# Performance work log

Measured on AMD Instinct MI355X. Metric: run time of the kernel, lower is better.

The kernel has to match this reference:

```python
import jax, jax.numpy as jnp
import numpy as np

B, S, D = 2, 2048, 2048
NH, NKV, HD = 32, 8, 64
RATIO = NH // NKV  # 4
EPS = 1e-6


def setup_inputs() -> dict:
    key = jax.random.key(0)
    ks = jax.random.split(key, 6)
    x = jax.random.normal(ks[0], (B, S, D), dtype=jnp.float32)
    # weights stored (in, out) so projection is x @ W
    wq = jax.random.normal(ks[1], (D, NH * HD), dtype=jnp.float32) * 0.02
    wk = jax.random.normal(ks[2], (D, NKV * HD), dtype=jnp.float32) * 0.02
    wv = jax.random.normal(ks[3], (D, NKV * HD), dtype=jnp.float32) * 0.02
    wo = jax.random.normal(ks[4], (NH * HD, D), dtype=jnp.float32) * 0.02
    q_scale = jnp.ones((HD,), dtype=jnp.float32)
    k_scale = jnp.ones((HD,), dtype=jnp.float32)
    # RoPE tables (S, HD): duplicated-half layout
    inv_freq = 1.0 / (10000.0 ** (np.arange(0, HD, 2, dtype=np.float32) / HD))
    t = np.arange(S, dtype=np.float32)
    freqs = np.outer(t, inv_freq)  # (S, HD/2)
    emb = np.concatenate([freqs, freqs], axis=-1)  # (S, HD)
    cos = jnp.asarray(np.cos(emb))
    sin = jnp.asarray(np.sin(emb))
    # causal mask: True above diagonal = masked
    mask = jnp.triu(jnp.ones((S, S), dtype=jnp.bool_), k=1)
    return {"x": x, "wq": wq, "wk": wk, "wv": wv, "wo": wo,
            "q_scale": q_scale, "k_scale": k_scale,
            "cos": cos, "sin": sin, "mask": mask}


def _rms_norm(x, scale):
    # Qwen3-compatible: compute in fp32, cast back
    idt = x.dtype
    xf = x.astype(jnp.float32)
    nx = xf * jax.lax.rsqrt(jnp.mean(xf * xf, axis=-1, keepdims=True) + EPS)
    return (nx * scale).astype(idt)


def _rope(x, cos, sin):
    # x: (b, h, s, hd); cos/sin: (s, hd)
    hd = x.shape[-1]
    x1, x2 = x[..., : hd // 2], x[..., hd // 2:]
    rot = jnp.concatenate([-x2, x1], axis=-1)
    return x * cos[None, None] + rot * sin[None, None]


def reference(x, wq, wk, wv, wo, q_scale, k_scale, cos, sin, mask):
    b, sl, _ = x.shape
    q = (x @ wq).reshape(b, sl, NH, HD).transpose(0, 2, 1, 3)    # (b, nh, s, hd)
    k = (x @ wk).reshape(b, sl, NKV, HD).transpose(0, 2, 1, 3)   # (b, nkv, s, hd)
    v = (x @ wv).reshape(b, sl, NKV, HD).transpose(0, 2, 1, 3)   # (b, nkv, s, hd)
    q = _rms_norm(q, q_scale)
    k = _rms_norm(k, k_scale)
    q = _rope(q, cos, sin)
    k = _rope(k, cos, sin)
    # GQA: repeat KV heads
    k = jnp.repeat(k, RATIO, axis=1)  # (b, nh, s, hd)
    v = jnp.repeat(v, RATIO, axis=1)
    scores = jnp.einsum('bhqd,bhkd->bhqk', q, k) / jnp.sqrt(jnp.float32(HD))
    scores = jnp.where(mask[None, None], jnp.finfo(scores.dtype).min, scores)
    attn = jax.nn.softmax(scores, axis=-1)
    out = jnp.einsum('bhqk,bhkd->bhqd', attn, v)
    out = out.transpose(0, 2, 1, 3).reshape(b, sl, NH * HD)
    return out @ wo
```

## Files before the change

### kernel.cpp

```cpp
#include <hip/hip_runtime.h>
#include <hip/hip_bf16.h>

typedef float f32x4 __attribute__((ext_vector_type(4)));
typedef float f32x16 __attribute__((ext_vector_type(16)));
typedef short s16x8 __attribute__((ext_vector_type(8)));
typedef unsigned short u16;
typedef unsigned short u16x8 __attribute__((ext_vector_type(8)));
typedef unsigned short u16x4 __attribute__((ext_vector_type(4)));
typedef unsigned int u32;
typedef unsigned int u32x4 __attribute__((ext_vector_type(4)));

#define MROWS 4096
#define NQKV  3072
#define DMODEL 2048

#define EXP2(x) __builtin_amdgcn_exp2f(x)

__device__ __forceinline__ u16 f2bf(float f) {
  __hip_bfloat16 h = __float2bfloat16(f);
  return __builtin_bit_cast(u16, h);
}
__device__ __forceinline__ float bf2f(u16 u) {
  __hip_bfloat16 h = __builtin_bit_cast(__hip_bfloat16, u);
  return __bfloat162float(h);
}

__device__ __forceinline__ u32 cvtpk(float a, float b) {
  u32 r;
  asm("v_cvt_pk_bf16_f32 %0, %1, %2" : "=v"(r) : "v"(a), "v"(b));
  return r;
}

typedef __attribute__((address_space(3))) unsigned int lds_u32_t;
typedef const __attribute__((address_space(1))) unsigned int glb_u32_t;
__device__ __forceinline__ void gload_lds16(const void* g, void* l) {
  __builtin_amdgcn_global_load_lds((glb_u32_t*)g, (lds_u32_t*)l, 16, 0, 0);
}

__global__ __launch_bounds__(256) void k_conv_x(const float* __restrict__ x, u16* __restrict__ o) {
  size_t i = ((size_t)blockIdx.x * 256 + threadIdx.x) * 4;
  float4 v = *(const float4*)(x + i);
  u16x4 r = { f2bf(v.x), f2bf(v.y), f2bf(v.z), f2bf(v.w) };
  *(u16x4*)(o + i) = r;
}

__global__ __launch_bounds__(256) void k_transw(const float* __restrict__ src, u16* __restrict__ dst,
                                                int N, int K) {
  __shared__ u16 t[64][68];
  int n0 = blockIdx.x * 64, k0 = blockIdx.y * 64;
  int tid = threadIdx.x;
#pragma unroll
  for (int r = 0; r < 4; ++r) {
    int k = r * 16 + (tid >> 4);
    int n = (tid & 15) * 4;
    float4 v = *(const float4*)(src + (size_t)(k0 + k) * N + n0 + n);
    t[n + 0][k] = f2bf(v.x);
    t[n + 1][k] = f2bf(v.y);
    t[n + 2][k] = f2bf(v.z);
    t[n + 3][k] = f2bf(v.w);
  }
  __syncthreads();
#pragma unroll
  for (int r = 0; r < 4; ++r) {
    int n = r * 16 + (tid >> 4);
    int k = (tid & 15) * 4;
    u16x4 o = { t[n][k], t[n][k + 1], t[n][k + 2], t[n][k + 3] };
    *(u16x4*)(dst + (size_t)(n0 + n) * K + k0 + k) = o;
  }
}

template <int BM, int BN, typename OutT>
__global__ __launch_bounds__(512, 2)
void k_gemm8(const u16* __restrict__ A, const u16* __restrict__ Bt,
             OutT* __restrict__ C, int M, int N, int K, int nbx) {
  static_assert(BM == 128, "A staging assumes one full 512x16B round");
  constexpr int WM = 2, WN = 4;
  constexpr int MF = BM / 16 / WM;
  constexpr int NF = BN / 16 / WN;
  __shared__ u16 sA[2][2][BM][32];
  __shared__ u16 sB[2][2][BN][32];
  const int nwg = gridDim.x;
  const int chunk = nwg >> 3;
  const int wg = (blockIdx.x & 7) * chunk + (blockIdx.x >> 3);
  const int m0 = (wg / nbx) * BM, n0 = (wg % nbx) * BN;
  const int tid = threadIdx.x;
  const int l = tid & 63;
  const int lo = l & 15, hi = l >> 4;
  const int wid = tid >> 6;
  const int wm = wid >> 2, wn = wid & 3;
  const int nkt = K >> 6;

  f32x4 acc[MF][NF] = {};

  auto STAGE = [&](int buf, int ks, int t) {
    {
      const int D = tid * 16;
      const int row = D >> 6;
      const int srcb = (D & 63) ^ (((row >> 1) & 3) << 4);
      gload_lds16((const char*)(A + (size_t)(m0 + row) * K + t * 64 + ks * 32) + srcb,
                  (char*)(&sA[buf][ks][0][0]) + D);
    }
#pragma unroll
    for (int i = 0; i < 2; ++i) {
      const int u = i * 512 + tid;
      if ((BN * 4) % 512 == 0 || u < BN * 4) {
        const int D = u * 16;
        const int row = D >> 6;
        const int srcb = (D & 63) ^ (((row >> 1) & 3) << 4);
        gload_lds16((const char*)(Bt + (size_t)(n0 + row) * K + t * 64 + ks * 32) + srcb,
                    (char*)(&sB[buf][ks][0][0]) + D);
      }
    }
  };

  auto WAITVM = [&]() {
    if constexpr (BN == 192) {
      if (wid < 4) asm volatile("s_waitcnt vmcnt(3)" ::: "memory");
      else         asm volatile("s_waitcnt vmcnt(2)" ::: "memory");
    } else {
      asm volatile("s_waitcnt vmcnt(3)" ::: "memory");
    }
  };

  auto PHASE = [&](int buf, int ks, int t1, bool st, int vmmode) {
    s16x8 a[MF], b[NF];
#pragma unroll
    for (int mf = 0; mf < MF; ++mf) {
      const int row = wm * (MF * 16) + mf * 16 + lo;
      a[mf] = *(const s16x8*)((const char*)(&sA[buf][ks][0][0]) + row * 64 +
                              ((hi * 16) ^ (((row >> 1) & 3) << 4)));
    }
#pragma unroll
    for (int nf = 0; nf < NF; ++nf) {
      const int row = wn * (NF * 16) + nf * 16 + lo;
      b[nf] = *(const s16x8*)((const char*)(&sB[buf][ks][0][0]) + row * 64 +
                              ((hi * 16) ^ (((row >> 1) & 3) << 4)));
    }
    if (st) STAGE(buf ^ 1, ks, t1);
    __builtin_amdgcn_sched_barrier(0);
    __builtin_amdgcn_s_barrier();
    asm volatile("s_waitcnt lgkmcnt(0)" ::: "memory");
    __builtin_amdgcn_sched_barrier(0);
    __builtin_amdgcn_s_setprio(1);
#pragma unroll
    for (int mf = 0; mf < MF; ++mf)
#pragma unroll
      for (int nf = 0; nf < NF; ++nf)
        acc[mf][nf] = __builtin_amdgcn_mfma_f32_16x16x32_bf16(a[mf], b[nf], acc[mf][nf], 0, 0, 0);
    __builtin_amdgcn_s_setprio(0);
    if (vmmode == 1) WAITVM();
    else if (vmmode == 2) asm volatile("s_waitcnt vmcnt(0)" ::: "memory");
    __builtin_amdgcn_sched_barrier(0);
    __builtin_amdgcn_s_barrier();
  };

  STAGE(0, 0, 0);
  STAGE(0, 1, 0);
  WAITVM();
  __builtin_amdgcn_s_barrier();

  for (int t = 0; t < nkt; ++t) {
    const int buf = t & 1;
    const bool st = (t + 1 < nkt);
    PHASE(buf, 0, t + 1, st, st ? 1 : 2);
    PHASE(buf, 1, t + 1, st, st ? 1 : 0);
  }

#pragma unroll
  for (int mf = 0; mf < MF; ++mf)
#pragma unroll
    for (int nf = 0; nf < NF; ++nf)
#pragma unroll
      for (int r = 0; r < 4; ++r) {
        const int row = m0 + wm * (MF * 16) + mf * 16 + hi * 4 + r;
        const int col = n0 + wn * (NF * 16) + nf * 16 + lo;
        if constexpr (__is_same(OutT, float)) C[(size_t)row * N + col] = acc[mf][nf][r];
        else                                  C[(size_t)row * N + col] = f2bf(acc[mf][nf][r]);
      }
}

__global__ __launch_bounds__(256) void k_normrope(const u16* __restrict__ qkv, u16* __restrict__ qn,
                                                  u16* __restrict__ kn, const float* __restrict__ qs,
                                                  const float* __restrict__ ksc,
                                                  const float* __restrict__ cosb,
                                                  const float* __restrict__ sinb) {
  int j = blockIdx.x * 4 + (threadIdx.x >> 6);
  int l = threadIdx.x & 63;
  bool isQ = j < MROWS * 32;
  int m, head, incol;
  if (isQ) { m = j >> 5; head = j & 31; incol = head * 64; }
  else     { int j2 = j - MROWS * 32; m = j2 >> 3; head = j2 & 7; incol = 2048 + head * 64; }
  float v = bf2f(qkv[(size_t)m * NQKV + incol + l]);
  float ss = v * v;
#pragma unroll
  for (int off = 1; off < 64; off <<= 1) ss += __shfl_xor(ss, off, 64);
  float inv = rsqrtf(ss * (1.0f / 64.0f) + 1e-6f);
  float nx = v * inv * (isQ ? qs[l] : ksc[l]);
  int s = m & 2047;
  float c = cosb[s * 64 + l], sn = sinb[s * 64 + l];
  float partner = __shfl_xor(nx, 32, 64);
  float rot = (l < 32) ? -partner : partner;
  float outv = nx * c + rot * sn;
  if (isQ) {
    outv *= 0.125f * 1.44269504088896f;
    qn[(size_t)m * 2048 + incol + l] = f2bf(outv);
  } else {
    kn[(size_t)m * 512 + head * 64 + l] = f2bf(outv);
  }
}

__global__ __launch_bounds__(256) void k_vtrans(const u16* __restrict__ qkv, u16* __restrict__ vt) {
  __shared__ u16 t[64][68];
  int s0 = blockIdx.x * 64;
  int bk = blockIdx.y;
  int tid = threadIdx.x;
#pragma unroll
  for (int r = 0; r < 4; ++r) {
    int s = r * 16 + (tid >> 4);
    int d = (tid & 15) * 4;
    u16x4 v = *(const u16x4*)(qkv + (size_t)((bk >> 3) * 2048 + s0 + s) * NQKV + 2560 + (bk & 7) * 64 + d);
    t[d + 0][s] = v[0];
    t[d + 1][s] = v[1];
    t[d + 2][s] = v[2];
    t[d + 3][s] = v[3];
  }
  __syncthreads();
#pragma unroll
  for (int r = 0; r < 4; ++r) {
    int d = r * 16 + (tid >> 4);
    int sl = (tid & 15) * 4;
    u16x4 o = { t[d][sl], t[d][sl + 1], t[d][sl + 2], t[d][sl + 3] };
    *(u16x4*)(vt + (size_t)(bk * 64 + d) * 2048 + s0 + sl) = o;
  }
}

__global__ __launch_bounds__(256) void k_attn(const u16* __restrict__ qn, const u16* __restrict__ kn,
                                              const u16* __restrict__ vt, u16* __restrict__ aout) {
  __shared__ char sK[2][64 * 128];
  __shared__ char sV[2][64 * 128];
  const int bid = blockIdx.x;
  const int kvh = bid & 7;
  const int b = (bid >> 3) & 1;
  const int hsub = (bid >> 4) & 3;
  const int a = (bid >> 6) & 3;
  const int k = bid >> 8;
  const int qt = (k == 0) ? 15 - a : (k == 1) ? 8 + a : (k == 2) ? 7 - a : a;
  const int h = kvh * 4 + hsub;
  const int tid = threadIdx.x, l = tid & 63, w = tid >> 6;
  const int l31 = l & 31, l5 = l >> 5;
  const int nkv = 2 * qt + 2;
  const u16* kbase = kn + (size_t)(b * 2048) * 512 + kvh * 64;
  const u16* vbase = vt + (size_t)((b * 8 + kvh) * 64) * 2048;
  const int srow = tid >> 3;
  const int scol = (tid & 7) * 8;
  const int sg_t = srow >> 4, sg_h = (srow >> 3) & 1, sg_j = srow & 7;
  const int krow0 = 32 * (sg_t >> 1) + 8 * ((sg_t & 1) * 2 + (sg_j >> 2)) + 4 * sg_h + (sg_j & 3);

  u16x8 krg0, krg1, vrg0, vrg1;
  auto issue = [&](int kv0) {
    krg0 = *(const u16x8*)(kbase + (size_t)(kv0 + srow) * 512 + scol);
    krg1 = *(const u16x8*)(kbase + (size_t)(kv0 + srow + 32) * 512 + scol);
    vrg0 = *(const u16x8*)(vbase + (size_t)srow * 2048 + kv0 + scol);
    vrg1 = *(const u16x8*)(vbase + (size_t)(srow + 32) * 2048 + kv0 + scol);
  };
  auto stash = [&](int buf) {
    const int cb = scol * 2;
    const int k0_ = krow0, k1_ = krow0 + 32;
    *(u16x8*)(sK[buf] + k0_ * 128 + (cb ^ ((k0_ & 7) << 4))) = krg0;
    *(u16x8*)(sK[buf] + k1_ * 128 + (cb ^ ((k1_ & 7) << 4))) = krg1;
    const int r0 = srow, r1 = srow + 32;
    *(u16x8*)(sV[buf] + r0 * 128 + (cb ^ ((r0 & 7) << 4))) = vrg0;
    *(u16x8*)(sV[buf] + r1 * 128 + (cb ^ ((r1 & 7) << 4))) = vrg1;
  };

  s16x8 qf[4];
  f32x16 O0, O1;
  float lst = 0.f;
  {
    const u16* qp = qn + (size_t)(b * 2048 + qt * 128 + w * 32 + l31) * 2048 + h * 64 + l5 * 8;
#pragma unroll
    for (int ki = 0; ki < 4; ++ki) qf[ki] = *(const s16x8*)(qp + ki * 16);
#pragma unroll
    for (int r = 0; r < 16; ++r) { O0[r] = 0.f; O1[r] = 0.f; }
  }

  issue(0);
  stash(0);
  for (int s = 0; s < nkv; ++s) {
    const int cur = s & 1;
    __syncthreads();
    if (s + 1 < nkv) issue((s + 1) * 64);
    f32x16 sc0, sc1;
#pragma unroll
    for (int r = 0; r < 16; ++r) { sc0[r] = 0.f; sc1[r] = 0.f; }
    __builtin_amdgcn_s_setprio(1);
#pragma unroll
    for (int ki = 0; ki < 4; ++ki) {
      const int cb = ki * 32 + l5 * 16;
      const int r0 = l31, r1 = 32 + l31;
      s16x8 a0 = *(const s16x8*)(sK[cur] + r0 * 128 + (cb ^ ((r0 & 7) << 4)));
      s16x8 a1 = *(const s16x8*)(sK[cur] + r1 * 128 + (cb ^ ((r1 & 7) << 4)));
      sc0 = __builtin_amdgcn_mfma_f32_32x32x16_bf16(a0, qf[ki], sc0, 0, 0, 0);
      sc1 = __builtin_amdgcn_mfma_f32_32x32x16_bf16(a1, qf[ki], sc1, 0, 0, 0);
    }
    __builtin_amdgcn_s_setprio(0);
    if (s >= 2 * qt) {
      const int qrow = qt * 128 + w * 32 + l31;
      const int kb0 = s * 64 + 8 * l5;
#pragma unroll
      for (int r = 0; r < 16; ++r) {
        const int klocal = 16 * (r >> 3) + 4 * ((r >> 2) & 1) + (r & 3);
        if (kb0 + klocal > qrow) sc0[r] = -1e30f;
        if (kb0 + 32 + klocal > qrow) sc1[r] = -1e30f;
      }
    }
    float rs = 0.f;
    u32 pk0[4][2], pk1[4][2];
#pragma unroll
    for (int g = 0; g < 4; ++g) {
      float a0 = EXP2(sc0[4*g+0]), a1 = EXP2(sc0[4*g+1]);
      float a2 = EXP2(sc0[4*g+2]), a3 = EXP2(sc0[4*g+3]);
      float b0 = EXP2(sc1[4*g+0]), b1 = EXP2(sc1[4*g+1]);
      float b2 = EXP2(sc1[4*g+2]), b3 = EXP2(sc1[4*g+3]);
      rs += ((a0 + a1) + (a2 + a3)) + ((b0 + b1) + (b2 + b3));
      pk0[g][0] = cvtpk(a0, a1);
      pk0[g][1] = cvtpk(a2, a3);
      pk1[g][0] = cvtpk(b0, b1);
      pk1[g][1] = cvtpk(b2, b3);
    }
    rs += __shfl_xor(rs, 32, 64);
    lst += rs;
#define PV_STEP(PK, GB, KB)                                                   \
    {                                                                         \
      u32x4 wv_ = { PK[GB][0], PK[GB][1], PK[GB+1][0], PK[GB+1][1] };         \
      s16x8 pb = __builtin_bit_cast(s16x8, wv_);                              \
      const int cb = (KB) * 32 + l5 * 16;                                     \
      const int rv0 = l31, rv1 = 32 + l31;                                    \
      s16x8 v0 = *(const s16x8*)(sV[cur] + rv0 * 128 + (cb ^ ((rv0 & 7) << 4))); \
      s16x8 v1 = *(const s16x8*)(sV[cur] + rv1 * 128 + (cb ^ ((rv1 & 7) << 4))); \
      __builtin_amdgcn_s_setprio(1);                                          \
      O0 = __builtin_amdgcn_mfma_f32_32x32x16_bf16(v0, pb, O0, 0, 0, 0);      \
      O1 = __builtin_amdgcn_mfma_f32_32x32x16_bf16(v1, pb, O1, 0, 0, 0);      \
      __builtin_amdgcn_s_setprio(0);                                          \
    }
    PV_STEP(pk0, 0, 0)
    PV_STEP(pk0, 2, 1)
    PV_STEP(pk1, 0, 2)
    PV_STEP(pk1, 2, 3)
#undef PV_STEP
    if (s + 1 < nkv) stash(cur ^ 1);
  }
  {
    const float inv = 1.0f / lst;
    const size_t rowoff = (size_t)(b * 2048 + qt * 128 + w * 32 + l31) * 2048 + h * 64;
#pragma unroll
    for (int g = 0; g < 4; ++g) {
      const int d0 = 8 * g + 4 * l5;
      u16x4 o0 = { f2bf(O0[4*g+0]*inv), f2bf(O0[4*g+1]*inv), f2bf(O0[4*g+2]*inv), f2bf(O0[4*g+3]*inv) };
      *(u16x4*)(aout + rowoff + d0) = o0;
      u16x4 o1 = { f2bf(O1[4*g+0]*inv), f2bf(O1[4*g+1]*inv), f2bf(O1[4*g+2]*inv), f2bf(O1[4*g+3]*inv) };
      *(u16x4*)(aout + rowoff + 32 + d0) = o1;
    }
  }
}

extern "C" void kernel_launch(void* const* d_in, const int* in_sizes, int n_in,
                              void* d_out, int out_size, void* d_ws, size_t ws_size,
                              hipStream_t stream) {
  (void)in_sizes; (void)n_in; (void)out_size; (void)ws_size;
  const float* x    = (const float*)d_in[0];
  const float* wq   = (const float*)d_in[1];
  const float* wk   = (const float*)d_in[2];
  const float* wv   = (const float*)d_in[3];
  const float* wo   = (const float*)d_in[4];
  const float* qs   = (const float*)d_in[5];
  const float* ksc  = (const float*)d_in[6];
  const float* cosb = (const float*)d_in[7];
  const float* sinb = (const float*)d_in[8];
  float* out = (float*)d_out;
  char* ws = (char*)d_ws;
  u16* xbf   = (u16*)(ws);
  u16* wqkvt = (u16*)(ws + 16777216);
  u16* wot   = (u16*)(ws + 29360128);
  u16* qkv   = (u16*)(ws + 37748736);
  u16* qn    = (u16*)(ws + 62914560);
  u16* kn    = (u16*)(ws + 79691776);
  u16* vt    = (u16*)(ws + 83886080);
  u16* aout  = (u16*)(ws + 88080384);

  k_conv_x<<<8192, 256, 0, stream>>>(x, xbf);
  k_transw<<<dim3(32, 32), 256, 0, stream>>>(wq, wqkvt, 2048, 2048);
  k_transw<<<dim3(8, 32), 256, 0, stream>>>(wk, wqkvt + (size_t)2048 * 2048, 512, 2048);
  k_transw<<<dim3(8, 32), 256, 0, stream>>>(wv, wqkvt + (size_t)2560 * 2048, 512, 2048);
  k_transw<<<dim3(32, 32), 256, 0, stream>>>(wo, wot, 2048, 2048);
  k_gemm8<128, 192, u16><<<512, 512, 0, stream>>>(xbf, wqkvt, qkv, MROWS, NQKV, 2048, 16);
  k_normrope<<<40960, 256, 0, stream>>>(qkv, qn, kn, qs, ksc, cosb, sinb);
  k_vtrans<<<dim3(32, 16), 256, 0, stream>>>(qkv, vt);
  k_attn<<<1024, 256, 0, stream>>>(qn, kn, vt, aout);
  k_gemm8<128, 256, float><<<256, 512, 0, stream>>>(aout, wot, out, MROWS, DMODEL, 2048, 8);
}
```

Baseline: 212.8 us.

## Split attention KV range across two wave groups and pair causal query tiles

The attention kernel now runs 512-thread blocks in which two groups of four waves each take alternating 64-row KV tiles, with a four-slot shared buffer. The two partial outputs and row sums are merged through shared memory before the write. Each block also handles a complementary pair of query tiles (15-p and p) so every block does the same total causal work, halving the grid. The aim is to shorten per-block serial KV loops and balance load, at the cost of an extra barrier per iteration and a merge step through shared memory.

```diff
diff --git a/kernel.cpp b/kernel.cpp
--- a/kernel.cpp
+++ b/kernel.cpp
@@ -234,133 +234,169 @@
   }
 }
 
-__global__ __launch_bounds__(256) void k_attn(const u16* __restrict__ qn, const u16* __restrict__ kn,
-                                              const u16* __restrict__ vt, u16* __restrict__ aout) {
-  __shared__ char sK[2][64 * 128];
-  __shared__ char sV[2][64 * 128];
+__global__ __launch_bounds__(512, 4) void k_attn(const u16* __restrict__ qn, const u16* __restrict__ kn,
+                                                 const u16* __restrict__ vt, u16* __restrict__ aout) {
+  __shared__ char sKV[4][2][64 * 128];
+  float* mO = (float*)&sKV[0][0][0];
+  float* mL = mO + 128 * 65;
   const int bid = blockIdx.x;
   const int kvh = bid & 7;
   const int b = (bid >> 3) & 1;
   const int hsub = (bid >> 4) & 3;
-  const int a = (bid >> 6) & 3;
-  const int k = bid >> 8;
-  const int qt = (k == 0) ? 15 - a : (k == 1) ? 8 + a : (k == 2) ? 7 - a : a;
+  const int p = bid >> 6;
   const int h = kvh * 4 + hsub;
-  const int tid = threadIdx.x, l = tid & 63, w = tid >> 6;
+  const int tid = threadIdx.x, l = tid & 63;
+  const int w = tid >> 6, qw = w & 3, half = w >> 2;
   const int l31 = l & 31, l5 = l >> 5;
-  const int nkv = 2 * qt + 2;
+  const int qtA = 15 - p, qtB = p;
   const u16* kbase = kn + (size_t)(b * 2048) * 512 + kvh * 64;
   const u16* vbase = vt + (size_t)((b * 8 + kvh) * 64) * 2048;
-  const int srow = tid >> 3;
-  const int scol = (tid & 7) * 8;
+  const int st = tid >> 8;
+  const int stid = tid & 255;
+  const int srow = stid >> 3;
+  const int scol = (stid & 7) * 8;
   const int sg_t = srow >> 4, sg_h = (srow >> 3) & 1, sg_j = srow & 7;
   const int krow0 = 32 * (sg_t >> 1) + 8 * ((sg_t & 1) * 2 + (sg_j >> 2)) + 4 * sg_h + (sg_j & 3);
 
   u16x8 krg0, krg1, vrg0, vrg1;
-  auto issue = [&](int kv0) {
+  int stbuf = 0;
+  auto issue = [&](int baset) {
+    const int tile = baset + st;
+    const int kv0 = tile * 64;
+    stbuf = tile & 3;
     krg0 = *(const u16x8*)(kbase + (size_t)(kv0 + srow) * 512 + scol);
     krg1 = *(const u16x8*)(kbase + (size_t)(kv0 + srow + 32) * 512 + scol);
     vrg0 = *(const u16x8*)(vbase + (size_t)srow * 2048 + kv0 + scol);
     vrg1 = *(const u16x8*)(vbase + (size_t)(srow + 32) * 2048 + kv0 + scol);
   };
-  auto stash = [&](int buf) {
+  auto stash = [&]() {
+    char* sK = sKV[stbuf][0];
+    char* sV = sKV[stbuf][1];
     const int cb = scol * 2;
     const int k0_ = krow0, k1_ = krow0 + 32;
-    *(u16x8*)(sK[buf] + k0_ * 128 + (cb ^ ((k0_ & 7) << 4))) = krg0;
-    *(u16x8*)(sK[buf] + k1_ * 128 + (cb ^ ((k1_ & 7) << 4))) = krg1;
+    *(u16x8*)(sK + k0_ * 128 + (cb ^ ((k0_ & 7) << 4))) = krg0;
+    *(u16x8*)(sK + k1_ * 128 + (cb ^ ((k1_ & 7) << 4))) = krg1;
     const int r0 = srow, r1 = srow + 32;
-    *(u16x8*)(sV[buf] + r0 * 128 + (cb ^ ((r0 & 7) << 4))) = vrg0;
-    *(u16x8*)(sV[buf] + r1 * 128 + (cb ^ ((r1 & 7) << 4))) = vrg1;
+    *(u16x8*)(sV + r0 * 128 + (cb ^ ((r0 & 7) << 4))) = vrg0;
+    *(u16x8*)(sV + r1 * 128 + (cb ^ ((r1 & 7) << 4))) = vrg1;
   };
 
   s16x8 qf[4];
   f32x16 O0, O1;
-  float lst = 0.f;
-  {
-    const u16* qp = qn + (size_t)(b * 2048 + qt * 128 + w * 32 + l31) * 2048 + h * 64 + l5 * 8;
-#pragma unroll
-    for (int ki = 0; ki < 4; ++ki) qf[ki] = *(const s16x8*)(qp + ki * 16);
-#pragma unroll
-    for (int r = 0; r < 16; ++r) { O0[r] = 0.f; O1[r] = 0.f; }
-  }
-
-  issue(0);
-  stash(0);
-  for (int s = 0; s < nkv; ++s) {
-    const int cur = s & 1;
+  float lst;
+
+  for (int mem = 0; mem < 2; ++mem) {
+    const int qt = mem ? qtB : qtA;
+    const int row = qw * 32 + l31;
+    {
+      const u16* qp = qn + (size_t)(b * 2048 + qt * 128 + row) * 2048 + h * 64 + l5 * 8;
+#pragma unroll
+      for (int ki = 0; ki < 4; ++ki) qf[ki] = *(const s16x8*)(qp + ki * 16);
+#pragma unroll
+      for (int r = 0; r < 16; ++r) { O0[r] = 0.f; O1[r] = 0.f; }
+      lst = 0.f;
+    }
+    issue(0);
+    stash();
     __syncthreads();
-    if (s + 1 < nkv) issue((s + 1) * 64);
-    f32x16 sc0, sc1;
-#pragma unroll
-    for (int r = 0; r < 16; ++r) { sc0[r] = 0.f; sc1[r] = 0.f; }
-    __builtin_amdgcn_s_setprio(1);
-#pragma unroll
-    for (int ki = 0; ki < 4; ++ki) {
-      const int cb = ki * 32 + l5 * 16;
-      const int r0 = l31, r1 = 32 + l31;
-      s16x8 a0 = *(const s16x8*)(sK[cur] + r0 * 128 + (cb ^ ((r0 & 7) << 4)));
-      s16x8 a1 = *(const s16x8*)(sK[cur] + r1 * 128 + (cb ^ ((r1 & 7) << 4)));
-      sc0 = __builtin_amdgcn_mfma_f32_32x32x16_bf16(a0, qf[ki], sc0, 0, 0, 0);
-      sc1 = __builtin_amdgcn_mfma_f32_32x32x16_bf16(a1, qf[ki], sc1, 0, 0, 0);
-    }
-    __builtin_amdgcn_s_setprio(0);
-    if (s >= 2 * qt) {
-      const int qrow = qt * 128 + w * 32 + l31;
-      const int kb0 = s * 64 + 8 * l5;
-#pragma unroll
-      for (int r = 0; r < 16; ++r) {
-        const int klocal = 16 * (r >> 3) + 4 * ((r >> 2) & 1) + (r & 3);
-        if (kb0 + klocal > qrow) sc0[r] = -1e30f;
-        if (kb0 + 32 + klocal > qrow) sc1[r] = -1e30f;
-      }
-    }
-    float rs = 0.f;
-    u32 pk0[4][2], pk1[4][2];
-#pragma unroll
-    for (int g = 0; g < 4; ++g) {
-      float a0 = EXP2(sc0[4*g+0]), a1 = EXP2(sc0[4*g+1]);
-      float a2 = EXP2(sc0[4*g+2]), a3 = EXP2(sc0[4*g+3]);
-      float b0 = EXP2(sc1[4*g+0]), b1 = EXP2(sc1[4*g+1]);
-      float b2 = EXP2(sc1[4*g+2]), b3 = EXP2(sc1[4*g+3]);
-      rs += ((a0 + a1) + (a2 + a3)) + ((b0 + b1) + (b2 + b3));
-      pk0[g][0] = cvtpk(a0, a1);
-      pk0[g][1] = cvtpk(a2, a3);
-      pk1[g][0] = cvtpk(b0, b1);
-      pk1[g][1] = cvtpk(b2, b3);
-    }
-    rs += __shfl_xor(rs, 32, 64);
-    lst += rs;
+    const int nss = qt + 1;
+    for (int i = 0; i < nss; ++i) {
+      const int T = 2 * i + half;
+      const char* sK = sKV[T & 3][0];
+      const char* sV = sKV[T & 3][1];
+      if (i + 1 < nss) issue(2 * i + 2);
+      f32x16 sc0, sc1;
+#pragma unroll
+      for (int r = 0; r < 16; ++r) { sc0[r] = 0.f; sc1[r] = 0.f; }
+      __builtin_amdgcn_s_setprio(1);
+#pragma unroll
+      for (int ki = 0; ki < 4; ++ki) {
+        const int cb = ki * 32 + l5 * 16;
+        const int r0 = l31, r1 = 32 + l31;
+        s16x8 a0 = *(const s16x8*)(sK + r0 * 128 + (cb ^ ((r0 & 7) << 4)));
+        s16x8 a1 = *(const s16x8*)(sK + r1 * 128 + (cb ^ ((r1 & 7) << 4)));
+        sc0 = __builtin_amdgcn_mfma_f32_32x32x16_bf16(a0, qf[ki], sc0, 0, 0, 0);
+        sc1 = __builtin_amdgcn_mfma_f32_32x32x16_bf16(a1, qf[ki], sc1, 0, 0, 0);
+      }
+      __builtin_amdgcn_s_setprio(0);
+      if (T >= 2 * qt) {
+        const int qrow = qt * 128 + row;
+        const int kb0 = T * 64 + 8 * l5;
+#pragma unroll
+        for (int r = 0; r < 16; ++r) {
+          const int klocal = 16 * (r >> 3) + 4 * ((r >> 2) & 1) + (r & 3);
+          if (kb0 + klocal > qrow) sc0[r] = -1e30f;
+          if (kb0 + 32 + klocal > qrow) sc1[r] = -1e30f;
+        }
+      }
+      float rs = 0.f;
+      u32 pk0[4][2], pk1[4][2];
+#pragma unroll
+      for (int g = 0; g < 4; ++g) {
+        float a0 = EXP2(sc0[4*g+0]), a1 = EXP2(sc0[4*g+1]);
+        float a2 = EXP2(sc0[4*g+2]), a3 = EXP2(sc0[4*g+3]);
+        float b0 = EXP2(sc1[4*g+0]), b1 = EXP2(sc1[4*g+1]);
+        float b2 = EXP2(sc1[4*g+2]), b3 = EXP2(sc1[4*g+3]);
+        rs += ((a0 + a1) + (a2 + a3)) + ((b0 + b1) + (b2 + b3));
+        pk0[g][0] = cvtpk(a0, a1);
+        pk0[g][1] = cvtpk(a2, a3);
+        pk1[g][0] = cvtpk(b0, b1);
+        pk1[g][1] = cvtpk(b2, b3);
+      }
+      rs += __shfl_xor(rs, 32, 64);
+      lst += rs;
 #define PV_STEP(PK, GB, KB)                                                   \
-    {                                                                         \
-      u32x4 wv_ = { PK[GB][0], PK[GB][1], PK[GB+1][0], PK[GB+1][1] };         \
-      s16x8 pb = __builtin_bit_cast(s16x8, wv_);                              \
-      const int cb = (KB) * 32 + l5 * 16;                                     \
-      const int rv0 = l31, rv1 = 32 + l31;                                    \
-      s16x8 v0 = *(const s16x8*)(sV[cur] + rv0 * 128 + (cb ^ ((rv0 & 7) << 4))); \
-      s16x8 v1 = *(const s16x8*)(sV[cur] + rv1 * 128 + (cb ^ ((rv1 & 7) << 4))); \
-      __builtin_amdgcn_s_setprio(1);                                          \
-      O0 = __builtin_amdgcn_mfma_f32_32x32x16_bf16(v0, pb, O0, 0, 0, 0);      \
-      O1 = __builtin_amdgcn_mfma_f32_32x32x16_bf16(v1, pb, O1, 0, 0, 0);      \
-      __builtin_amdgcn_s_setprio(0);                                          \
-    }
-    PV_STEP(pk0, 0, 0)
-    PV_STEP(pk0, 2, 1)
-    PV_STEP(pk1, 0, 2)
-    PV_STEP(pk1, 2, 3)
+      {                                                                       \
+        u32x4 wv_ = { PK[GB][0], PK[GB][1], PK[GB+1][0], PK[GB+1][1] };       \
+        s16x8 pb = __builtin_bit_cast(s16x8, wv_);                            \
+        const int cb = (KB) * 32 + l5 * 16;                                   \
+        const int rv0 = l31, rv1 = 32 + l31;                                  \
+        s16x8 v0 = *(const s16x8*)(sV + rv0 * 128 + (cb ^ ((rv0 & 7) << 4))); \
+        s16x8 v1 = *(const s16x8*)(sV + rv1 * 128 + (cb ^ ((rv1 & 7) << 4))); \
+        __builtin_amdgcn_s_setprio(1);                                        \
+        O0 = __builtin_amdgcn_mfma_f32_32x32x16_bf16(v0, pb, O0, 0, 0, 0);    \
+        O1 = __builtin_amdgcn_mfma_f32_32x32x16_bf16(v1, pb, O1, 0, 0, 0);    \
+        __builtin_amdgcn_s_setprio(0);                                        \
+      }
+      PV_STEP(pk0, 0, 0)
+      PV_STEP(pk0, 2, 1)
+      PV_STEP(pk1, 0, 2)
+      PV_STEP(pk1, 2, 3)
 #undef PV_STEP
-    if (s + 1 < nkv) stash(cur ^ 1);
-  }
-  {
-    const float inv = 1.0f / lst;
-    const size_t rowoff = (size_t)(b * 2048 + qt * 128 + w * 32 + l31) * 2048 + h * 64;
-#pragma unroll
-    for (int g = 0; g < 4; ++g) {
-      const int d0 = 8 * g + 4 * l5;
-      u16x4 o0 = { f2bf(O0[4*g+0]*inv), f2bf(O0[4*g+1]*inv), f2bf(O0[4*g+2]*inv), f2bf(O0[4*g+3]*inv) };
-      *(u16x4*)(aout + rowoff + d0) = o0;
-      u16x4 o1 = { f2bf(O1[4*g+0]*inv), f2bf(O1[4*g+1]*inv), f2bf(O1[4*g+2]*inv), f2bf(O1[4*g+3]*inv) };
-      *(u16x4*)(aout + rowoff + 32 + d0) = o1;
-    }
+      if (i + 1 < nss) stash();
+      __syncthreads();
+    }
+    if (half == 1) {
+#pragma unroll
+      for (int g = 0; g < 4; ++g)
+#pragma unroll
+        for (int j = 0; j < 4; ++j) {
+          const int d = 8 * g + 4 * l5 + j;
+          mO[row * 65 + d] = O0[4*g+j];
+          mO[row * 65 + 32 + d] = O1[4*g+j];
+        }
+      if (l5 == 0) mL[row] = lst;
+    }
+    __syncthreads();
+    if (half == 0) {
+      const float inv = 1.0f / (lst + mL[row]);
+      const size_t rowoff = (size_t)(b * 2048 + qt * 128 + row) * 2048 + h * 64;
+#pragma unroll
+      for (int g = 0; g < 4; ++g) {
+        const int d0 = 8 * g + 4 * l5;
+        u16x4 o0 = { f2bf((O0[4*g+0] + mO[row*65+d0+0]) * inv),
+                     f2bf((O0[4*g+1] + mO[row*65+d0+1]) * inv),
+                     f2bf((O0[4*g+2] + mO[row*65+d0+2]) * inv),
+                     f2bf((O0[4*g+3] + mO[row*65+d0+3]) * inv) };
+        *(u16x4*)(aout + rowoff + d0) = o0;
+        u16x4 o1 = { f2bf((O1[4*g+0] + mO[row*65+32+d0+0]) * inv),
+                     f2bf((O1[4*g+1] + mO[row*65+32+d0+1]) * inv),
+                     f2bf((O1[4*g+2] + mO[row*65+32+d0+2]) * inv),
+                     f2bf((O1[4*g+3] + mO[row*65+32+d0+3]) * inv) };
+        *(u16x4*)(aout + rowoff + 32 + d0) = o1;
+      }
+    }
+    __syncthreads();
   }
 }
 
@@ -396,6 +432,6 @@
   k_gemm8<128, 192, u16><<<512, 512, 0, stream>>>(xbf, wqkvt, qkv, MROWS, NQKV, 2048, 16);
   k_normrope<<<40960, 256, 0, stream>>>(qkv, qn, kn, qs, ksc, cosb, sinb);
   k_vtrans<<<dim3(32, 16), 256, 0, stream>>>(qkv, vt);
-  k_attn<<<1024, 256, 0, stream>>>(qn, kn, vt, aout);
+  k_attn<<<512, 512, 0, stream>>>(qn, kn, vt, aout);
   k_gemm8<128, 256, float><<<256, 512, 0, stream>>>(aout, wot, out, MROWS, DMODEL, 2048, 8);
 }
```

Measured after the change: 214.9 us. About the same (+1.0%).
